# Kernel optimization log

Hardware: AMD Instinct MI355X
Metric: run time of the kernel (lower is better)

The kernel has to match this reference:

```python
import jax, jax.numpy as jnp
import numpy as np


def setup_inputs() -> dict:
    key = jax.random.key(0)
    k1, k2, k3, k4 = jax.random.split(key, 4)
    B, IN, OUT, K = 1024, 1024, 1024, 100
    return {
        "x": jax.random.normal(k1, (B, IN), dtype=jnp.float32),
        "eps": jax.random.normal(k2, (K, IN, OUT), dtype=jnp.float32),
        "weights_m": jax.random.normal(k3, (IN, OUT), dtype=jnp.float32),
        "weights_s": jax.random.normal(k4, (IN, OUT), dtype=jnp.float32),
    }


def reference(x, eps, weights_m, weights_s):
    # Reparameterized Gaussian weight samples: [K, in, out]
    sampled = eps * jax.nn.softplus(weights_s) + weights_m
    # einsum('ij,kjl->kil'): preds [K, B, out]
    preds = jnp.einsum('ij,kjl->kil', x, sampled)
    return preds.mean(0)
```

## Files before the change

kernel.cpp:

```cpp
#include <hip/hip_runtime.h>
#include <cmath>

#define KSAMP 100
#define DIN   1024
#define DOUT  1024
#define DB    1024

typedef float f4 __attribute__((ext_vector_type(4)));

__global__ __launch_bounds__(256) void weff_kernel(
    const f4* __restrict__ eps,
    const f4* __restrict__ wm,
    const f4* __restrict__ ws,
    f4* __restrict__ weff)
{
    const int idx = blockIdx.x * blockDim.x + threadIdx.x;
    const int n4 = (DIN * DOUT) / 4;

    f4 acc0 = {0.f, 0.f, 0.f, 0.f};
    f4 acc1 = {0.f, 0.f, 0.f, 0.f};
    const f4* p = eps + idx;
    #pragma unroll 10
    for (int k = 0; k < KSAMP; k += 2) {
        f4 e0 = __builtin_nontemporal_load(p);
        f4 e1 = __builtin_nontemporal_load(p + n4);
        p += 2 * n4;
        acc0 += e0;
        acc1 += e1;
    }
    f4 sum = acc0 + acc1;

    f4 s = ws[idx];
    f4 m = wm[idx];
    const float invK = 1.0f / (float)KSAMP;

    f4 sp;
    sp.x = fmaxf(s.x, 0.f) + log1pf(expf(-fabsf(s.x)));
    sp.y = fmaxf(s.y, 0.f) + log1pf(expf(-fabsf(s.y)));
    sp.z = fmaxf(s.z, 0.f) + log1pf(expf(-fabsf(s.z)));
    sp.w = fmaxf(s.w, 0.f) + log1pf(expf(-fabsf(s.w)));

    f4 o;
    o.x = fmaf(sum.x * invK, sp.x, m.x);
    o.y = fmaf(sum.y * invK, sp.y, m.y);
    o.z = fmaf(sum.z * invK, sp.z, m.z);
    o.w = fmaf(sum.w * invK, sp.w, m.w);
    weff[idx] = o;
}

#define BM 128
#define BN 128
#define BK 8
#define KSPLIT 8

__global__ __launch_bounds__(256, 2) void sgemm_splitk(
    const float* __restrict__ A,
    const float* __restrict__ B,
    float* __restrict__ P)
{
    __shared__ float As[BK][BM];
    __shared__ float Bs[BK][BN];

    const int bx = blockIdx.x, by = blockIdx.y, kz = blockIdx.z;
    const int tid = threadIdx.x;
    const int tx = tid & 15;
    const int ty = tid >> 4;

    const int kc = DIN / KSPLIT;
    const int k_begin = kz * kc;

    const int arow = tid >> 1;
    const int acol = (tid & 1) * 4;
    const int brow = tid >> 5;
    const int bcol = (tid & 31) * 4;

    const float* Aptr = &A[(size_t)(by * BM + arow) * DIN + k_begin + acol];
    const float* Bptr = &B[(size_t)(k_begin + brow) * DOUT + bx * BN + bcol];

    float acc[8][8];
    #pragma unroll
    for (int i = 0; i < 8; ++i)
        #pragma unroll
        for (int j = 0; j < 8; ++j) acc[i][j] = 0.f;

    float4 a = *(const float4*)Aptr;
    float4 b = *(const float4*)Bptr;

    const int niter = kc / BK;
    for (int it = 0; it < niter; ++it) {
        __syncthreads();
        As[acol + 0][arow] = a.x;
        As[acol + 1][arow] = a.y;
        As[acol + 2][arow] = a.z;
        As[acol + 3][arow] = a.w;
        *(float4*)&Bs[brow][bcol] = b;
        __syncthreads();

        if (it + 1 < niter) {
            a = *(const float4*)(Aptr + (it + 1) * BK);
            b = *(const float4*)(Bptr + (size_t)(it + 1) * BK * DOUT);
        }

        #pragma unroll
        for (int kk = 0; kk < BK; ++kk) {
            float4 a0 = *(const float4*)&As[kk][ty * 8];
            float4 a1 = *(const float4*)&As[kk][ty * 8 + 4];
            float4 b0 = *(const float4*)&Bs[kk][tx * 4];
            float4 b1 = *(const float4*)&Bs[kk][64 + tx * 4];
            const float ar[8] = {a0.x, a0.y, a0.z, a0.w, a1.x, a1.y, a1.z, a1.w};
            const float br[8] = {b0.x, b0.y, b0.z, b0.w, b1.x, b1.y, b1.z, b1.w};
            #pragma unroll
            for (int i = 0; i < 8; ++i)
                #pragma unroll
                for (int j = 0; j < 8; ++j)
                    acc[i][j] = fmaf(ar[i], br[j], acc[i][j]);
        }
    }

    float* Pz = P + (size_t)kz * DB * DOUT;
    #pragma unroll
    for (int i = 0; i < 8; ++i) {
        const int r = by * BM + ty * 8 + i;
        float* prow = &Pz[(size_t)r * DOUT + bx * BN];
        *(f4*)&prow[tx * 4]      = (f4){acc[i][0], acc[i][1], acc[i][2], acc[i][3]};
        *(f4*)&prow[64 + tx * 4] = (f4){acc[i][4], acc[i][5], acc[i][6], acc[i][7]};
    }
}

__global__ __launch_bounds__(256) void reduce_kernel(
    const f4* __restrict__ P, f4* __restrict__ out)
{
    const int idx = blockIdx.x * blockDim.x + threadIdx.x;
    const int n4 = (DB * DOUT) / 4;
    f4 s = P[idx];
    #pragma unroll
    for (int z = 1; z < KSPLIT; ++z) {
        s += P[(size_t)z * n4 + idx];
    }
    out[idx] = s;
}

extern "C" void kernel_launch(void* const* d_in, const int* in_sizes, int n_in,
                              void* d_out, int out_size, void* d_ws, size_t ws_size,
                              hipStream_t stream) {
    const float* x   = (const float*)d_in[0];
    const float* eps = (const float*)d_in[1];
    const float* wm  = (const float*)d_in[2];
    const float* ws  = (const float*)d_in[3];

    float* weff     = (float*)d_ws;
    float* partials = (float*)d_ws + (size_t)DIN * DOUT;

    weff_kernel<<<(DIN * DOUT / 4) / 256, 256, 0, stream>>>(
        (const f4*)eps, (const f4*)wm, (const f4*)ws, (f4*)weff);

    sgemm_splitk<<<dim3(DOUT / BN, DB / BM, KSPLIT), 256, 0, stream>>>(
        x, weff, partials);

    reduce_kernel<<<(DB * DOUT / 4) / 256, 256, 0, stream>>>(
        (const f4*)partials, (f4*)d_out);
}
```

Baseline: 584.9 us.

## Replace FP32 split-K SGEMM with split-bf16 MFMA GEMM and transposed weights

Swaps the FP32 SIMT split-K GEMM and its reduction kernel for a GEMM on bf16 MFMA instructions. Each FP32 operand is split into a bf16 high part and a bf16 low part, and three MFMA products are summed (hi*hi, hi*lo, lo*hi) to approximate FP32 accuracy. The weff kernel now also converts x into the hi/lo split, and a new transpose kernel lays the weights out K-contiguous for the MFMA loads. This removes the FP32 FMA work and the partial-sum traffic. In exchange it adds a transpose pass, the GEMM loads operands straight from global memory without LDS tiling, and precision is slightly lower than true FP32.

```diff
diff --git a/kernel.cpp b/kernel.cpp
--- a/kernel.cpp
+++ b/kernel.cpp
@@ -6,16 +6,40 @@
 #define DOUT  1024
 #define DB    1024
 
-typedef float f4 __attribute__((ext_vector_type(4)));
+typedef float f4    __attribute__((ext_vector_type(4)));
+typedef float f32x4 __attribute__((ext_vector_type(4)));
+typedef __bf16 bf16x8 __attribute__((ext_vector_type(8)));
+typedef unsigned short us4v __attribute__((ext_vector_type(4)));
+
+static __device__ __forceinline__ unsigned short f2bf(float x) {
+    unsigned u = __float_as_uint(x);
+    u += 0x7fffu + ((u >> 16) & 1u);
+    return (unsigned short)(u >> 16);
+}
+static __device__ __forceinline__ float bf2f(unsigned short h) {
+    return __uint_as_float(((unsigned)h) << 16);
+}
 
 __global__ __launch_bounds__(256) void weff_kernel(
     const f4* __restrict__ eps,
     const f4* __restrict__ wm,
     const f4* __restrict__ ws,
-    f4* __restrict__ weff)
+    const f4* __restrict__ x,
+    us4v* __restrict__ wh, us4v* __restrict__ wl,
+    us4v* __restrict__ xh, us4v* __restrict__ xl)
 {
     const int idx = blockIdx.x * blockDim.x + threadIdx.x;
     const int n4 = (DIN * DOUT) / 4;
+
+    {
+        f4 xv = x[idx];
+        us4v hi, lo;
+        hi.x = f2bf(xv.x); lo.x = f2bf(xv.x - bf2f(hi.x));
+        hi.y = f2bf(xv.y); lo.y = f2bf(xv.y - bf2f(hi.y));
+        hi.z = f2bf(xv.z); lo.z = f2bf(xv.z - bf2f(hi.z));
+        hi.w = f2bf(xv.w); lo.w = f2bf(xv.w - bf2f(hi.w));
+        xh[idx] = hi; xl[idx] = lo;
+    }
 
     f4 acc0 = {0.f, 0.f, 0.f, 0.f};
     f4 acc1 = {0.f, 0.f, 0.f, 0.f};
@@ -40,104 +64,124 @@
     sp.z = fmaxf(s.z, 0.f) + log1pf(expf(-fabsf(s.z)));
     sp.w = fmaxf(s.w, 0.f) + log1pf(expf(-fabsf(s.w)));
 
-    f4 o;
-    o.x = fmaf(sum.x * invK, sp.x, m.x);
-    o.y = fmaf(sum.y * invK, sp.y, m.y);
-    o.z = fmaf(sum.z * invK, sp.z, m.z);
-    o.w = fmaf(sum.w * invK, sp.w, m.w);
-    weff[idx] = o;
-}
-
-#define BM 128
-#define BN 128
-#define BK 8
-#define KSPLIT 8
-
-__global__ __launch_bounds__(256, 2) void sgemm_splitk(
-    const float* __restrict__ A,
-    const float* __restrict__ B,
-    float* __restrict__ P)
-{
-    __shared__ float As[BK][BM];
-    __shared__ float Bs[BK][BN];
-
-    const int bx = blockIdx.x, by = blockIdx.y, kz = blockIdx.z;
-    const int tid = threadIdx.x;
-    const int tx = tid & 15;
-    const int ty = tid >> 4;
-
-    const int kc = DIN / KSPLIT;
-    const int k_begin = kz * kc;
-
-    const int arow = tid >> 1;
-    const int acol = (tid & 1) * 4;
-    const int brow = tid >> 5;
-    const int bcol = (tid & 31) * 4;
-
-    const float* Aptr = &A[(size_t)(by * BM + arow) * DIN + k_begin + acol];
-    const float* Bptr = &B[(size_t)(k_begin + brow) * DOUT + bx * BN + bcol];
-
-    float acc[8][8];
+    f4 w;
+    w.x = fmaf(sum.x * invK, sp.x, m.x);
+    w.y = fmaf(sum.y * invK, sp.y, m.y);
+    w.z = fmaf(sum.z * invK, sp.z, m.z);
+    w.w = fmaf(sum.w * invK, sp.w, m.w);
+
+    us4v hi, lo;
+    hi.x = f2bf(w.x); lo.x = f2bf(w.x - bf2f(hi.x));
+    hi.y = f2bf(w.y); lo.y = f2bf(w.y - bf2f(hi.y));
+    hi.z = f2bf(w.z); lo.z = f2bf(w.z - bf2f(hi.z));
+    hi.w = f2bf(w.w); lo.w = f2bf(w.w - bf2f(hi.w));
+    wh[idx] = hi; wl[idx] = lo;
+}
+
+__device__ __forceinline__ void transpose_one(
+    const unsigned short* __restrict__ S, unsigned short* __restrict__ D,
+    unsigned short (*T)[66], int bi, int bj, int t)
+{
+    const int il = t >> 2;
+    const int j0 = (t & 3) * 16;
+    const uint4* p = (const uint4*)&S[(size_t)(bi * 64 + il) * DOUT + bj * 64 + j0];
+    uint4 v0 = p[0], v1 = p[1];
+    unsigned q[8] = {v0.x, v0.y, v0.z, v0.w, v1.x, v1.y, v1.z, v1.w};
     #pragma unroll
-    for (int i = 0; i < 8; ++i)
-        #pragma unroll
-        for (int j = 0; j < 8; ++j) acc[i][j] = 0.f;
-
-    float4 a = *(const float4*)Aptr;
-    float4 b = *(const float4*)Bptr;
-
-    const int niter = kc / BK;
-    for (int it = 0; it < niter; ++it) {
-        __syncthreads();
-        As[acol + 0][arow] = a.x;
-        As[acol + 1][arow] = a.y;
-        As[acol + 2][arow] = a.z;
-        As[acol + 3][arow] = a.w;
-        *(float4*)&Bs[brow][bcol] = b;
-        __syncthreads();
-
-        if (it + 1 < niter) {
-            a = *(const float4*)(Aptr + (it + 1) * BK);
-            b = *(const float4*)(Bptr + (size_t)(it + 1) * BK * DOUT);
-        }
-
-        #pragma unroll
-        for (int kk = 0; kk < BK; ++kk) {
-            float4 a0 = *(const float4*)&As[kk][ty * 8];
-            float4 a1 = *(const float4*)&As[kk][ty * 8 + 4];
-            float4 b0 = *(const float4*)&Bs[kk][tx * 4];
-            float4 b1 = *(const float4*)&Bs[kk][64 + tx * 4];
-            const float ar[8] = {a0.x, a0.y, a0.z, a0.w, a1.x, a1.y, a1.z, a1.w};
-            const float br[8] = {b0.x, b0.y, b0.z, b0.w, b1.x, b1.y, b1.z, b1.w};
-            #pragma unroll
-            for (int i = 0; i < 8; ++i)
-                #pragma unroll
-                for (int j = 0; j < 8; ++j)
-                    acc[i][j] = fmaf(ar[i], br[j], acc[i][j]);
-        }
-    }
-
-    float* Pz = P + (size_t)kz * DB * DOUT;
+    for (int c = 0; c < 8; ++c) {
+        T[j0 + 2 * c    ][il] = (unsigned short)(q[c] & 0xffffu);
+        T[j0 + 2 * c + 1][il] = (unsigned short)(q[c] >> 16);
+    }
+    __syncthreads();
+    const int ol = t >> 2;
+    const int i0 = (t & 3) * 16;
+    const unsigned* Tp = (const unsigned*)&T[ol][i0];
+    unsigned r[8];
     #pragma unroll
-    for (int i = 0; i < 8; ++i) {
-        const int r = by * BM + ty * 8 + i;
-        float* prow = &Pz[(size_t)r * DOUT + bx * BN];
-        *(f4*)&prow[tx * 4]      = (f4){acc[i][0], acc[i][1], acc[i][2], acc[i][3]};
-        *(f4*)&prow[64 + tx * 4] = (f4){acc[i][4], acc[i][5], acc[i][6], acc[i][7]};
-    }
-}
-
-__global__ __launch_bounds__(256) void reduce_kernel(
-    const f4* __restrict__ P, f4* __restrict__ out)
-{
-    const int idx = blockIdx.x * blockDim.x + threadIdx.x;
-    const int n4 = (DB * DOUT) / 4;
-    f4 s = P[idx];
+    for (int s2 = 0; s2 < 8; ++s2) r[s2] = Tp[s2];
+    uint4 o0 = {r[0], r[1], r[2], r[3]};
+    uint4 o1 = {r[4], r[5], r[6], r[7]};
+    uint4* dp = (uint4*)&D[(size_t)(bj * 64 + ol) * DIN + bi * 64 + i0];
+    dp[0] = o0; dp[1] = o1;
+}
+
+__global__ __launch_bounds__(256) void transpose_kernel(
+    const unsigned short* __restrict__ Wh, const unsigned short* __restrict__ Wl,
+    unsigned short* __restrict__ WTh, unsigned short* __restrict__ WTl)
+{
+    __shared__ unsigned short T[64][66];
+    const int t = threadIdx.x;
+    const int bi = blockIdx.y, bj = blockIdx.x;
+    transpose_one(Wh, WTh, T, bi, bj, t);
+    __syncthreads();
+    transpose_one(Wl, WTl, T, bi, bj, t);
+}
+
+#define MFMA16(a, b, c) __builtin_amdgcn_mfma_f32_16x16x32_bf16((a), (b), (c), 0, 0, 0)
+
+__global__ __launch_bounds__(256) void gemm_mfma(
+    const unsigned short* __restrict__ Xh, const unsigned short* __restrict__ Xl,
+    const unsigned short* __restrict__ WTh, const unsigned short* __restrict__ WTl,
+    float* __restrict__ Out)
+{
+    const int tid  = threadIdx.x;
+    const int lane = tid & 63, wave = tid >> 6;
+    const int wr = wave >> 1, wc = wave & 1;
+    const int l15 = lane & 15, lq = lane >> 4;
+    const int row0 = blockIdx.y * 64 + wr * 32;
+    const int col0 = blockIdx.x * 64 + wc * 32;
+    const int kq = lq * 8;
+
+    const unsigned short* pa0h = &Xh [(size_t)(row0 + l15)      * DIN + kq];
+    const unsigned short* pa1h = &Xh [(size_t)(row0 + 16 + l15) * DIN + kq];
+    const unsigned short* pa0l = &Xl [(size_t)(row0 + l15)      * DIN + kq];
+    const unsigned short* pa1l = &Xl [(size_t)(row0 + 16 + l15) * DIN + kq];
+    const unsigned short* pb0h = &WTh[(size_t)(col0 + l15)      * DIN + kq];
+    const unsigned short* pb1h = &WTh[(size_t)(col0 + 16 + l15) * DIN + kq];
+    const unsigned short* pb0l = &WTl[(size_t)(col0 + l15)      * DIN + kq];
+    const unsigned short* pb1l = &WTl[(size_t)(col0 + 16 + l15) * DIN + kq];
+
+    f32x4 acc00 = {0.f, 0.f, 0.f, 0.f};
+    f32x4 acc01 = {0.f, 0.f, 0.f, 0.f};
+    f32x4 acc10 = {0.f, 0.f, 0.f, 0.f};
+    f32x4 acc11 = {0.f, 0.f, 0.f, 0.f};
+
+    #pragma unroll 4
+    for (int k0 = 0; k0 < DIN; k0 += 32) {
+        bf16x8 ah0 = *(const bf16x8*)(pa0h + k0);
+        bf16x8 ah1 = *(const bf16x8*)(pa1h + k0);
+        bf16x8 al0 = *(const bf16x8*)(pa0l + k0);
+        bf16x8 al1 = *(const bf16x8*)(pa1l + k0);
+        bf16x8 bh0 = *(const bf16x8*)(pb0h + k0);
+        bf16x8 bh1 = *(const bf16x8*)(pb1h + k0);
+        bf16x8 bl0 = *(const bf16x8*)(pb0l + k0);
+        bf16x8 bl1 = *(const bf16x8*)(pb1l + k0);
+
+        acc00 = MFMA16(ah0, bh0, acc00);
+        acc01 = MFMA16(ah0, bh1, acc01);
+        acc10 = MFMA16(ah1, bh0, acc10);
+        acc11 = MFMA16(ah1, bh1, acc11);
+
+        acc00 = MFMA16(ah0, bl0, acc00);
+        acc01 = MFMA16(ah0, bl1, acc01);
+        acc10 = MFMA16(ah1, bl0, acc10);
+        acc11 = MFMA16(ah1, bl1, acc11);
+
+        acc00 = MFMA16(al0, bh0, acc00);
+        acc01 = MFMA16(al0, bh1, acc01);
+        acc10 = MFMA16(al1, bh0, acc10);
+        acc11 = MFMA16(al1, bh1, acc11);
+    }
+
     #pragma unroll
-    for (int z = 1; z < KSPLIT; ++z) {
-        s += P[(size_t)z * n4 + idx];
-    }
-    out[idx] = s;
+    for (int r = 0; r < 4; ++r) {
+        const size_t ro0 = (size_t)(row0 + lq * 4 + r) * DOUT;
+        const size_t ro1 = (size_t)(row0 + 16 + lq * 4 + r) * DOUT;
+        Out[ro0 + col0 + l15]      = acc00[r];
+        Out[ro0 + col0 + 16 + l15] = acc01[r];
+        Out[ro1 + col0 + l15]      = acc10[r];
+        Out[ro1 + col0 + 16 + l15] = acc11[r];
+    }
 }
 
 extern "C" void kernel_launch(void* const* d_in, const int* in_sizes, int n_in,
@@ -148,15 +192,20 @@
     const float* wm  = (const float*)d_in[2];
     const float* ws  = (const float*)d_in[3];
 
-    float* weff     = (float*)d_ws;
-    float* partials = (float*)d_ws + (size_t)DIN * DOUT;
+    unsigned short* base = (unsigned short*)d_ws;
+    const size_t NE = (size_t)DIN * DOUT;
+    unsigned short* xh  = base + 0 * NE;
+    unsigned short* xl  = base + 1 * NE;
+    unsigned short* wh  = base + 2 * NE;
+    unsigned short* wl  = base + 3 * NE;
+    unsigned short* wth = base + 4 * NE;
+    unsigned short* wtl = base + 5 * NE;
 
     weff_kernel<<<(DIN * DOUT / 4) / 256, 256, 0, stream>>>(
-        (const f4*)eps, (const f4*)wm, (const f4*)ws, (f4*)weff);
-
-    sgemm_splitk<<<dim3(DOUT / BN, DB / BM, KSPLIT), 256, 0, stream>>>(
-        x, weff, partials);
-
-    reduce_kernel<<<(DB * DOUT / 4) / 256, 256, 0, stream>>>(
-        (const f4*)partials, (f4*)d_out);
-}
+        (const f4*)eps, (const f4*)wm, (const f4*)ws, (const f4*)x,
+        (us4v*)wh, (us4v*)wl, (us4v*)xh, (us4v*)xl);
+
+    transpose_kernel<<<dim3(16, 16), 256, 0, stream>>>(wh, wl, wth, wtl);
+
+    gemm_mfma<<<dim3(16, 16), 256, 0, stream>>>(xh, xl, wth, wtl, (float*)d_out);
+}
```

Result: faster. 572.0 us (-2.2%).
